# Kernel optimization log

Hardware: AMD Instinct MI355X
Metric: run time of the kernel (lower is better)

## Reference

```python
import jax, jax.numpy as jnp
import numpy as np

STRIDE, PAD, DIL = 1, 1, 1


def setup_inputs() -> dict:
    key = jax.random.key(0)
    k1, k2, k3, k4, k5 = jax.random.split(key, 5)
    N, Cin, H, W = 8, 256, 64, 64
    Cout, K = 256, 3
    x = jax.random.normal(k1, (N, Cin, H, W), dtype=jnp.float32)
    offset = jax.random.normal(k2, (N, 2 * K * K, H, W), dtype=jnp.float32)
    mask = jax.random.uniform(k3, (N, K * K, H, W), dtype=jnp.float32)
    weight = jax.random.normal(k4, (Cout, Cin, K, K), dtype=jnp.float32) * 0.02
    bias = jax.random.normal(k5, (Cout,), dtype=jnp.float32)
    return {"x": x, "offset": offset, "mask": mask, "weight": weight, "bias": bias}


def _gather(im_flat, idx):
    # im_flat: (N, Goff, Cg, H*W); idx: (N, Goff, KK, Ho, Wo) int32
    # -> (N, Goff, Cg, KK, Ho, Wo)
    f = lambda imf, ix: imf[:, ix]
    return jax.vmap(jax.vmap(f))(im_flat, idx)


def _deform_conv2d(x, offset, mask, weight, bias):
    N, Cin, H, W = x.shape
    Cout, Cin_g, Kh, Kw = weight.shape
    KK = Kh * Kw
    Goff = offset.shape[1] // (2 * KK)
    Ho = (H + 2 * PAD - (DIL * (Kh - 1) + 1)) // STRIDE + 1
    Wo = (W + 2 * PAD - (DIL * (Kw - 1) + 1)) // STRIDE + 1

    # base sampling grid per kernel tap: (KK, Ho, Wo)
    py = (jnp.arange(Kh)[:, None] * DIL + jnp.arange(Ho)[None, :] * STRIDE - PAD).astype(jnp.float32)
    px = (jnp.arange(Kw)[:, None] * DIL + jnp.arange(Wo)[None, :] * STRIDE - PAD).astype(jnp.float32)
    y_base = jnp.broadcast_to(py[:, None, :, None], (Kh, Kw, Ho, Wo)).reshape(KK, Ho, Wo)
    x_base = jnp.broadcast_to(px[None, :, None, :], (Kh, Kw, Ho, Wo)).reshape(KK, Ho, Wo)

    off = offset.reshape(N, Goff, KK, 2, Ho, Wo)  # [...,0]=dy, [...,1]=dx
    ys = y_base[None, None] + off[:, :, :, 0]  # (N, Goff, KK, Ho, Wo)
    xs = x_base[None, None] + off[:, :, :, 1]

    Cg = Cin // Goff
    im_flat = x.reshape(N, Goff, Cg, H * W)

    y0 = jnp.floor(ys)
    x0 = jnp.floor(xs)
    acc = jnp.zeros((N, Goff, Cg, KK, Ho, Wo), dtype=x.dtype)
    for dy in (0.0, 1.0):
        for dx in (0.0, 1.0):
            yi = y0 + dy
            xi = x0 + dx
            wgt = (1.0 - jnp.abs(ys - yi)) * (1.0 - jnp.abs(xs - xi))
            valid = (yi >= 0) & (yi < H) & (xi >= 0) & (xi < W)
            idx = (jnp.clip(yi, 0, H - 1) * W + jnp.clip(xi, 0, W - 1)).astype(jnp.int32)
            g = _gather(im_flat, idx)  # (N,Goff,Cg,KK,Ho,Wo)
            acc = acc + g * (wgt * valid.astype(x.dtype))[:, :, None]

    m = mask.reshape(N, Goff, KK, Ho, Wo)
    sampled = acc * m[:, :, None]  # DCNv2 modulation

    # grouped conv accumulate as GEMM over (Cin_g*KK)
    gw = Cin // Cin_g
    cols = sampled.reshape(N, gw, Cin_g * KK, Ho * Wo)
    wflat = weight.reshape(gw, Cout // gw, Cin_g * KK)
    out = jnp.einsum('goc,ngcl->ngol', wflat, cols).reshape(N, Cout, Ho, Wo)
    return out + bias[None, :, None, None]


def reference(x, offset, mask, weight, bias):
    return _deform_conv2d(x, offset, mask, weight, bias)
```

## Files before the change

### kernel.cpp

```cpp
#include <hip/hip_runtime.h>
#include <stdint.h>

typedef unsigned int u32;
typedef unsigned short u16;
typedef float f32x4 __attribute__((ext_vector_type(4)));
typedef __fp16 h16x2 __attribute__((ext_vector_type(2)));
typedef _Float16 f16x8 __attribute__((ext_vector_type(8)));

#define NB   8
#define CIN  256
#define HH   64
#define WW   64
#define HW   4096
#define COUT 256

__device__ __forceinline__ u32 pkh(float lo, float hi) {
  h16x2 h = __builtin_amdgcn_cvt_pkrtz(lo, hi);
  return __builtin_bit_cast(u32, h);
}
union HU { u32 u; h16x2 h; };

__global__ __launch_bounds__(256) void prep_w(const float* __restrict__ w,
                                              u16* __restrict__ W2f) {
  int t = blockIdx.x * 256 + threadIdx.x;
  int lane = t & 63;
  int tile = (t >> 6) & 15;
  int cc = (t >> 10) & 7;
  int kk = t >> 13;
  int co = ((tile >> 2) << 6) + ((tile & 3) << 4) + (lane & 15);
  int c0 = (cc << 5) + ((lane >> 4) << 3);
  u32 pk[4];
#pragma unroll
  for (int jj = 0; jj < 4; ++jj) {
    float v0 = w[((size_t)co * CIN + c0 + 2 * jj) * 9 + kk];
    float v1 = w[((size_t)co * CIN + c0 + 2 * jj + 1) * 9 + kk];
    pk[jj] = pkh(v0, v1);
  }
  *(uint4*)(W2f + (size_t)t * 8) = *(uint4*)pk;
}

__global__ __launch_bounds__(256) void prep_x(const float* __restrict__ x,
                                              u32* __restrict__ xT) {
  __shared__ u32 tile[64][129];
  int b = blockIdx.x;
  int n = b >> 6;
  int hw0 = (b & 63) << 6;
  int t = threadIdx.x;
  int hw = t & 63;
  const float* xb = x + (size_t)n * CIN * HW + hw0 + hw;
  int cbase = (t >> 6) * 2;
  for (int citer = 0; citer < 32; ++citer) {
    int c = (citer << 3) + cbase;
    float v0 = xb[(size_t)c * HW];
    float v1 = xb[(size_t)(c + 1) * HW];
    tile[hw][c >> 1] = pkh(v0, v1);
  }
  __syncthreads();
  u32* outp = xT + ((size_t)(n * HW + hw0)) * 128;
  int cp = t & 127;
  int hb = t >> 7;
  for (int it = 0; it < 32; ++it) {
    int hwl = (it << 1) + hb;
    outp[(size_t)hwl * 128 + cp] = tile[hwl][cp];
  }
}

#define BSTRIDE 264

__global__ __launch_bounds__(512, 4) void dcn_main(
    const float* __restrict__ offset, const float* __restrict__ mask,
    const float* __restrict__ bias, const u16* __restrict__ xT,
    const u16* __restrict__ W2f, float* __restrict__ out) {
  __shared__ __align__(16) u16 Bs[64 * BSTRIDE];
  __shared__ __align__(16) float4 swl[576];
  __shared__ __align__(8)  ushort4 sol[576];

  int bid = blockIdx.x;
  int n = bid & 7;
  int ho = bid >> 3;
  int t = threadIdx.x;
  int lane = t & 63;
  int w = t >> 6;

  for (int i = t; i < 576; i += 512) {
    int kk = i >> 6, p = i & 63;
    int ky = kk / 3, kx = kk - ky * 3;
    int sp = (ho << 6) + p;
    float dy = offset[(((size_t)n * 18 + kk * 2 + 0) << 12) + sp];
    float dx = offset[(((size_t)n * 18 + kk * 2 + 1) << 12) + sp];
    float m  = mask  [(((size_t)n * 9  + kk) << 12) + sp];
    float ys = (float)(ky + ho - 1) + dy;
    float xs = (float)(kx + p  - 1) + dx;
    float y0f = floorf(ys), x0f = floorf(xs);
    float fy = ys - y0f, fx = xs - x0f;
    int y0 = (int)y0f, x0 = (int)x0f;
    int y1 = y0 + 1, x1 = x0 + 1;
    float vy0 = (y0 >= 0 && y0 < HH) ? 1.f : 0.f;
    float vy1 = (y1 >= 0 && y1 < HH) ? 1.f : 0.f;
    float vx0 = (x0 >= 0 && x0 < WW) ? 1.f : 0.f;
    float vx1 = (x1 >= 0 && x1 < WW) ? 1.f : 0.f;
    float4 wv;
    wv.x = (1.f - fy) * (1.f - fx) * m * vy0 * vx0;
    wv.y = (1.f - fy) * fx * m * vy0 * vx1;
    wv.z = fy * (1.f - fx) * m * vy1 * vx0;
    wv.w = fy * fx * m * vy1 * vx1;
    int iy0 = min(max(y0, 0), HH - 1), iy1 = min(max(y1, 0), HH - 1);
    int ix0 = min(max(x0, 0), WW - 1), ix1 = min(max(x1, 0), WW - 1);
    ushort4 pv;
    pv.x = (u16)((iy0 << 6) + ix0);
    pv.y = (u16)((iy0 << 6) + ix1);
    pv.z = (u16)((iy1 << 6) + ix0);
    pv.w = (u16)((iy1 << 6) + ix1);
    swl[i] = wv;
    sol[i] = pv;
  }
  __syncthreads();

  f32x4 acc[2][4];
#pragma unroll
  for (int a = 0; a < 2; ++a)
#pragma unroll
    for (int b2 = 0; b2 < 4; ++b2) acc[a][b2] = {0.f, 0.f, 0.f, 0.f};

  const char* xTn = (const char*)xT + ((size_t)n * HW << 9);
  int ml = lane & 15, q = lane >> 4;
  int hwid = t >> 5;
  int l32 = t & 31;
  int tile0 = ((w >> 1) << 2) + ((w & 1) << 1);

#define CORNER(P, WT) do {                                             \
    uint4 qv = *(const uint4*)(bch + ((int)(P) << 9));                 \
    float wt = (WT);                                                   \
    HU h0, h1, h2, h3;                                                 \
    h0.u = qv.x; h1.u = qv.y; h2.u = qv.z; h3.u = qv.w;                \
    s0 = __builtin_fmaf((float)h0.h.x, wt, s0);                        \
    s1 = __builtin_fmaf((float)h0.h.y, wt, s1);                        \
    s2 = __builtin_fmaf((float)h1.h.x, wt, s2);                        \
    s3 = __builtin_fmaf((float)h1.h.y, wt, s3);                        \
    s4 = __builtin_fmaf((float)h2.h.x, wt, s4);                        \
    s5 = __builtin_fmaf((float)h2.h.y, wt, s5);                        \
    s6 = __builtin_fmaf((float)h3.h.x, wt, s6);                        \
    s7 = __builtin_fmaf((float)h3.h.y, wt, s7);                        \
  } while (0)

  for (int kk = 0; kk < 9; ++kk) {
#pragma unroll
    for (int i = 0; i < 4; ++i) {
      int px = (i << 4) + hwid;
      const float4 wv = swl[(kk << 6) + px];
      const ushort4 pv = sol[(kk << 6) + px];
      const char* bch = xTn + (l32 << 4);
      float s0=0.f,s1=0.f,s2=0.f,s3=0.f,s4=0.f,s5=0.f,s6=0.f,s7=0.f;
      CORNER(pv.x, wv.x);
      CORNER(pv.y, wv.y);
      CORNER(pv.z, wv.z);
      CORNER(pv.w, wv.w);
      uint4 pkd;
      pkd.x = pkh(s0, s1); pkd.y = pkh(s2, s3);
      pkd.z = pkh(s4, s5); pkd.w = pkh(s6, s7);
      *(uint4*)((char*)Bs + px * (BSTRIDE * 2) + (l32 << 4)) = pkd;
    }
    __syncthreads();

#pragma unroll 2
    for (int cc = 0; cc < 8; ++cc) {
      f16x8 af[2], bf[4];
      const u16* abase = W2f + (((size_t)(kk * 8 + cc) << 4) << 6 << 3);
#pragma unroll
      for (int mt = 0; mt < 2; ++mt)
        af[mt] = *(const f16x8*)(abase + ((((tile0 + mt) << 6) + lane) << 3));
#pragma unroll
      for (int nt = 0; nt < 4; ++nt)
        bf[nt] = *(const f16x8*)((const char*)Bs +
                 ((nt << 4) + ml) * (BSTRIDE * 2) + (cc << 6) + (q << 4));
#pragma unroll
      for (int mt = 0; mt < 2; ++mt)
#pragma unroll
        for (int nt = 0; nt < 4; ++nt)
          acc[mt][nt] = __builtin_amdgcn_mfma_f32_16x16x32_f16(af[mt], bf[nt],
                                                               acc[mt][nt], 0, 0, 0);
    }
    __syncthreads();
  }

  size_t obase = ((size_t)n * COUT) * HW + ((size_t)ho << 6);
#pragma unroll
  for (int mt = 0; mt < 2; ++mt) {
#pragma unroll
    for (int r = 0; r < 4; ++r) {
      int co = (w << 5) + (mt << 4) + (q << 2) + r;
      float bv = bias[co];
#pragma unroll
      for (int nt = 0; nt < 4; ++nt) {
        int wo = (nt << 4) + ml;
        out[obase + (size_t)co * HW + wo] = acc[mt][nt][r] + bv;
      }
    }
  }
}

extern "C" void kernel_launch(void* const* d_in, const int* in_sizes, int n_in,
                              void* d_out, int out_size, void* d_ws, size_t ws_size,
                              hipStream_t stream) {
  const float* x      = (const float*)d_in[0];
  const float* offset = (const float*)d_in[1];
  const float* mask   = (const float*)d_in[2];
  const float* weight = (const float*)d_in[3];
  const float* bias   = (const float*)d_in[4];
  float* out = (float*)d_out;

  u16* xT  = (u16*)d_ws;
  u16* W2f = (u16*)((char*)d_ws + (size_t)NB * HW * CIN * 2);

  prep_x<<<512, 256, 0, stream>>>(x, (u32*)xT);
  prep_w<<<288, 256, 0, stream>>>(weight, W2f);
  dcn_main<<<512, 512, 0, stream>>>(offset, mask, bias, xT, W2f, out);
}
```

Baseline: 150.9 us.

## Double-buffer sampled tile to overlap gather with MFMA, merge prep kernels

The sampled-column tile in shared memory is now double-buffered. Gathering for the next kernel tap is interleaved with the MFMA loop over the current tap, leaving one barrier per tap instead of two. The two prep kernels are merged into one launch, with vectorized x loads and a weight repack that reads contiguous weights. Bilinear weights are stored as fp16 pairs to shrink LDS. The trade-off is more LDS per block, which may lower occupancy, and bilinear-weight precision drops to fp16.

```diff
diff --git a/kernel.cpp b/kernel.cpp
--- a/kernel.cpp
+++ b/kernel.cpp
@@ -6,6 +6,7 @@
 typedef float f32x4 __attribute__((ext_vector_type(4)));
 typedef __fp16 h16x2 __attribute__((ext_vector_type(2)));
 typedef _Float16 f16x8 __attribute__((ext_vector_type(8)));
+typedef float f4u __attribute__((ext_vector_type(4), aligned(4)));
 
 #define NB   8
 #define CIN  256
@@ -13,6 +14,7 @@
 #define WW   64
 #define HW   4096
 #define COUT 256
+#define BSTR 264
 
 __device__ __forceinline__ u32 pkh(float lo, float hi) {
   h16x2 h = __builtin_amdgcn_cvt_pkrtz(lo, hi);
@@ -20,59 +22,70 @@
 }
 union HU { u32 u; h16x2 h; };
 
-__global__ __launch_bounds__(256) void prep_w(const float* __restrict__ w,
-                                              u16* __restrict__ W2f) {
-  int t = blockIdx.x * 256 + threadIdx.x;
-  int lane = t & 63;
-  int tile = (t >> 6) & 15;
-  int cc = (t >> 10) & 7;
-  int kk = t >> 13;
-  int co = ((tile >> 2) << 6) + ((tile & 3) << 4) + (lane & 15);
-  int c0 = (cc << 5) + ((lane >> 4) << 3);
-  u32 pk[4];
-#pragma unroll
-  for (int jj = 0; jj < 4; ++jj) {
-    float v0 = w[((size_t)co * CIN + c0 + 2 * jj) * 9 + kk];
-    float v1 = w[((size_t)co * CIN + c0 + 2 * jj + 1) * 9 + kk];
-    pk[jj] = pkh(v0, v1);
-  }
-  *(uint4*)(W2f + (size_t)t * 8) = *(uint4*)pk;
-}
-
-__global__ __launch_bounds__(256) void prep_x(const float* __restrict__ x,
-                                              u32* __restrict__ xT) {
-  __shared__ u32 tile[64][129];
+__global__ __launch_bounds__(256) void prep_all(const float* __restrict__ x,
+                                                const float* __restrict__ wgt,
+                                                u32* __restrict__ xT,
+                                                u32* __restrict__ W2f32) {
   int b = blockIdx.x;
-  int n = b >> 6;
-  int hw0 = (b & 63) << 6;
   int t = threadIdx.x;
-  int hw = t & 63;
-  const float* xb = x + (size_t)n * CIN * HW + hw0 + hw;
-  int cbase = (t >> 6) * 2;
-  for (int citer = 0; citer < 32; ++citer) {
-    int c = (citer << 3) + cbase;
-    float v0 = xb[(size_t)c * HW];
-    float v1 = xb[(size_t)(c + 1) * HW];
-    tile[hw][c >> 1] = pkh(v0, v1);
-  }
-  __syncthreads();
-  u32* outp = xT + ((size_t)(n * HW + hw0)) * 128;
-  int cp = t & 127;
-  int hb = t >> 7;
-  for (int it = 0; it < 32; ++it) {
-    int hwl = (it << 1) + hb;
-    outp[(size_t)hwl * 128 + cp] = tile[hwl][cp];
-  }
-}
-
-#define BSTRIDE 264
+  if (b < 512) {
+    __shared__ u32 tile[64][129];
+    int n = b >> 6, hw0 = (b & 63) << 6;
+    int hw4 = (t & 15) << 2;
+    int cp0 = t >> 4;
+    const float* xb = x + (size_t)n * CIN * HW + hw0 + hw4;
+#pragma unroll
+    for (int it = 0; it < 8; ++it) {
+      int cp = (it << 4) + cp0;
+      int c = cp << 1;
+      f4u v0 = *(const f4u*)(xb + (size_t)c * HW);
+      f4u v1 = *(const f4u*)(xb + (size_t)(c + 1) * HW);
+      tile[hw4 + 0][cp] = pkh(v0.x, v1.x);
+      tile[hw4 + 1][cp] = pkh(v0.y, v1.y);
+      tile[hw4 + 2][cp] = pkh(v0.z, v1.z);
+      tile[hw4 + 3][cp] = pkh(v0.w, v1.w);
+    }
+    __syncthreads();
+    u32* outp = xT + ((size_t)(n * HW + hw0)) * 128;
+    int cp = t & 127, hb = t >> 7;
+#pragma unroll
+    for (int it = 0; it < 32; ++it) {
+      int hwl = (it << 1) + hb;
+      outp[(size_t)hwl * 128 + cp] = tile[hwl][cp];
+    }
+  } else {
+    int tt = (b - 512) * 256 + t;
+    int cp = tt & 127, co = tt >> 7;
+    int c = cp << 1;
+    const float* p = wgt + ((size_t)co * CIN + c) * 9;
+    f4u q0 = *(const f4u*)(p + 0);
+    f4u q1 = *(const f4u*)(p + 4);
+    f4u q2 = *(const f4u*)(p + 8);
+    f4u q3 = *(const f4u*)(p + 12);
+    float e16 = p[16], e17 = p[17];
+    float a0[9], a1[9];
+    a0[0]=q0.x; a0[1]=q0.y; a0[2]=q0.z; a0[3]=q0.w;
+    a0[4]=q1.x; a0[5]=q1.y; a0[6]=q1.z; a0[7]=q1.w; a0[8]=q2.x;
+    a1[0]=q2.y; a1[1]=q2.z; a1[2]=q2.w;
+    a1[3]=q3.x; a1[4]=q3.y; a1[5]=q3.z; a1[6]=q3.w; a1[7]=e16; a1[8]=e17;
+    int cc = c >> 5;
+    int j = (c >> 1) & 3;
+    int lane = (co & 15) | (((c >> 3) & 3) << 4);
+    int tile_ = ((co >> 6) << 2) | ((co >> 4) & 3);
+#pragma unroll
+    for (int kk = 0; kk < 9; ++kk) {
+      int frag = (kk * 8 + cc) * 16 + tile_;
+      W2f32[(size_t)frag * 256 + lane * 4 + j] = pkh(a0[kk], a1[kk]);
+    }
+  }
+}
 
 __global__ __launch_bounds__(512, 4) void dcn_main(
     const float* __restrict__ offset, const float* __restrict__ mask,
     const float* __restrict__ bias, const u16* __restrict__ xT,
     const u16* __restrict__ W2f, float* __restrict__ out) {
-  __shared__ __align__(16) u16 Bs[64 * BSTRIDE];
-  __shared__ __align__(16) float4 swl[576];
+  __shared__ __align__(16) u16 Bs[2][64 * BSTR];
+  __shared__ __align__(8)  uint2 swl[576];
   __shared__ __align__(8)  ushort4 sol[576];
 
   int bid = blockIdx.x;
@@ -99,11 +112,10 @@
     float vy1 = (y1 >= 0 && y1 < HH) ? 1.f : 0.f;
     float vx0 = (x0 >= 0 && x0 < WW) ? 1.f : 0.f;
     float vx1 = (x1 >= 0 && x1 < WW) ? 1.f : 0.f;
-    float4 wv;
-    wv.x = (1.f - fy) * (1.f - fx) * m * vy0 * vx0;
-    wv.y = (1.f - fy) * fx * m * vy0 * vx1;
-    wv.z = fy * (1.f - fx) * m * vy1 * vx0;
-    wv.w = fy * fx * m * vy1 * vx1;
+    float w0 = (1.f - fy) * (1.f - fx) * m * vy0 * vx0;
+    float w1 = (1.f - fy) * fx * m * vy0 * vx1;
+    float w2 = fy * (1.f - fx) * m * vy1 * vx0;
+    float w3 = fy * fx * m * vy1 * vx1;
     int iy0 = min(max(y0, 0), HH - 1), iy1 = min(max(y1, 0), HH - 1);
     int ix0 = min(max(x0, 0), WW - 1), ix1 = min(max(x1, 0), WW - 1);
     ushort4 pv;
@@ -111,7 +123,7 @@
     pv.y = (u16)((iy0 << 6) + ix1);
     pv.z = (u16)((iy1 << 6) + ix0);
     pv.w = (u16)((iy1 << 6) + ix1);
-    swl[i] = wv;
+    swl[i] = make_uint2(pkh(w0, w1), pkh(w2, w3));
     sol[i] = pv;
   }
   __syncthreads();
@@ -127,6 +139,7 @@
   int hwid = t >> 5;
   int l32 = t & 31;
   int tile0 = ((w >> 1) << 2) + ((w & 1) << 1);
+  const char* bch = xTn + (l32 << 4);
 
 #define CORNER(P, WT) do {                                             \
     uint4 qv = *(const uint4*)(bch + ((int)(P) << 9));                 \
@@ -143,42 +156,53 @@
     s7 = __builtin_fmaf((float)h3.h.y, wt, s7);                        \
   } while (0)
 
+  auto build = [&](int kk, int i, int buf) {
+    int px = (i << 4) + hwid;
+    uint2 wu = swl[(kk << 6) + px];
+    ushort4 pv = sol[(kk << 6) + px];
+    HU ha, hb; ha.u = wu.x; hb.u = wu.y;
+    float w0 = (float)ha.h.x, w1 = (float)ha.h.y;
+    float w2 = (float)hb.h.x, w3 = (float)hb.h.y;
+    float s0=0.f,s1=0.f,s2=0.f,s3=0.f,s4=0.f,s5=0.f,s6=0.f,s7=0.f;
+    CORNER(pv.x, w0);
+    CORNER(pv.y, w1);
+    CORNER(pv.z, w2);
+    CORNER(pv.w, w3);
+    uint4 pkd;
+    pkd.x = pkh(s0, s1); pkd.y = pkh(s2, s3);
+    pkd.z = pkh(s4, s5); pkd.w = pkh(s6, s7);
+    *(uint4*)((char*)&Bs[buf][0] + px * (BSTR * 2) + (l32 << 4)) = pkd;
+  };
+
+#pragma unroll
+  for (int i = 0; i < 4; ++i) build(0, i, 0);
+  __syncthreads();
+
+#pragma unroll 1
   for (int kk = 0; kk < 9; ++kk) {
-#pragma unroll
-    for (int i = 0; i < 4; ++i) {
-      int px = (i << 4) + hwid;
-      const float4 wv = swl[(kk << 6) + px];
-      const ushort4 pv = sol[(kk << 6) + px];
-      const char* bch = xTn + (l32 << 4);
-      float s0=0.f,s1=0.f,s2=0.f,s3=0.f,s4=0.f,s5=0.f,s6=0.f,s7=0.f;
-      CORNER(pv.x, wv.x);
-      CORNER(pv.y, wv.y);
-      CORNER(pv.z, wv.z);
-      CORNER(pv.w, wv.w);
-      uint4 pkd;
-      pkd.x = pkh(s0, s1); pkd.y = pkh(s2, s3);
-      pkd.z = pkh(s4, s5); pkd.w = pkh(s6, s7);
-      *(uint4*)((char*)Bs + px * (BSTRIDE * 2) + (l32 << 4)) = pkd;
-    }
-    __syncthreads();
-
-#pragma unroll 2
-    for (int cc = 0; cc < 8; ++cc) {
-      f16x8 af[2], bf[4];
-      const u16* abase = W2f + (((size_t)(kk * 8 + cc) << 4) << 6 << 3);
-#pragma unroll
-      for (int mt = 0; mt < 2; ++mt)
-        af[mt] = *(const f16x8*)(abase + ((((tile0 + mt) << 6) + lane) << 3));
-#pragma unroll
-      for (int nt = 0; nt < 4; ++nt)
-        bf[nt] = *(const f16x8*)((const char*)Bs +
-                 ((nt << 4) + ml) * (BSTRIDE * 2) + (cc << 6) + (q << 4));
-#pragma unroll
-      for (int mt = 0; mt < 2; ++mt)
+    int cur = kk & 1;
+#pragma unroll
+    for (int g = 0; g < 4; ++g) {
+      if (kk < 8) build(kk + 1, g, cur ^ 1);
+#pragma unroll
+      for (int c2 = 0; c2 < 2; ++c2) {
+        int cc = (g << 1) | c2;
+        f16x8 af[2], bf[4];
+#pragma unroll
+        for (int mt = 0; mt < 2; ++mt)
+          af[mt] = *(const f16x8*)(W2f +
+                   (((size_t)((kk * 8 + cc) * 16 + tile0 + mt)) << 9) + (lane << 3));
 #pragma unroll
         for (int nt = 0; nt < 4; ++nt)
-          acc[mt][nt] = __builtin_amdgcn_mfma_f32_16x16x32_f16(af[mt], bf[nt],
-                                                               acc[mt][nt], 0, 0, 0);
+          bf[nt] = *(const f16x8*)((const char*)&Bs[cur][0] +
+                   ((nt << 4) + ml) * (BSTR * 2) + (cc << 6) + (q << 4));
+#pragma unroll
+        for (int mt = 0; mt < 2; ++mt)
+#pragma unroll
+          for (int nt = 0; nt < 4; ++nt)
+            acc[mt][nt] = __builtin_amdgcn_mfma_f32_16x16x32_f16(af[mt], bf[nt],
+                                                                 acc[mt][nt], 0, 0, 0);
+      }
     }
     __syncthreads();
   }
@@ -212,7 +236,6 @@
   u16* xT  = (u16*)d_ws;
   u16* W2f = (u16*)((char*)d_ws + (size_t)NB * HW * CIN * 2);
 
-  prep_x<<<512, 256, 0, stream>>>(x, (u32*)xT);
-  prep_w<<<288, 256, 0, stream>>>(weight, W2f);
+  prep_all<<<640, 256, 0, stream>>>(x, weight, (u32*)xT, (u32*)W2f);
   dcn_main<<<512, 512, 0, stream>>>(offset, mask, bias, xT, W2f, out);
 }
```

Measured after the change: 148.8 us. Within noise of the previous version (-1.4%).
